# Performance work log

Measured on AMD Instinct MI355X. Metric: run time of the kernel, lower is better.

The kernel has to match this reference:

```python
import jax, jax.numpy as jnp
import numpy as np

EMBED_DIM = 1024
NUM_HEADS = 16
HEAD_DIM = EMBED_DIM // NUM_HEADS
CHUNK_SIZE = 10
LEFT_CONTEXT = 25
RIGHT_CONTEXT = 0
NEG_INF = -1e30  # stands in for float('-inf') additive mask, safe under softmax


def chunk_attention_mask(seq_len: int) -> jnp.ndarray:
    """Vectorized version of the per-row Python loop mask builder.
    Row i may attend to: its own chunk [chunk_start, chunk_end), the left
    context [i-left_context, chunk_start), and the right context
    [chunk_end, i+right_context+1)."""
    i = jnp.arange(seq_len)[:, None]
    j = jnp.arange(seq_len)[None, :]
    chunk_start = (i // CHUNK_SIZE) * CHUNK_SIZE
    chunk_end = jnp.minimum(chunk_start + CHUNK_SIZE, seq_len)
    in_chunk = (j >= chunk_start) & (j < chunk_end)
    in_left = (j >= i - LEFT_CONTEXT) & (j < chunk_start)
    in_right = (j >= chunk_end) & (j < jnp.minimum(seq_len, i + RIGHT_CONTEXT + 1))
    allowed = in_chunk | in_left | in_right
    return jnp.where(allowed, 0.0, NEG_INF).astype(jnp.float32)


def setup_inputs() -> dict:
    key = jax.random.key(0)
    ks = jax.random.split(key, 9)
    B, S, E = 2, 2048, EMBED_DIM
    s = 1.0 / np.sqrt(E)
    return {
        "hidden_states": jax.random.normal(ks[0], (B, S, E), jnp.float32),
        "Wq": jax.random.normal(ks[1], (E, E), jnp.float32) * s,
        "bq": jax.random.normal(ks[2], (E,), jnp.float32) * 0.02,
        "Wk": jax.random.normal(ks[3], (E, E), jnp.float32) * s,
        "bk": jax.random.normal(ks[4], (E,), jnp.float32) * 0.02,
        "Wv": jax.random.normal(ks[5], (E, E), jnp.float32) * s,
        "bv": jax.random.normal(ks[6], (E,), jnp.float32) * 0.02,
        "Wo": jax.random.normal(ks[7], (E, E), jnp.float32) * s,
        "bo": jax.random.normal(ks[8], (E,), jnp.float32) * 0.02,
    }


def reference(hidden_states, Wq, bq, Wk, bk, Wv, bv, Wo, bo):
    B, S, E = hidden_states.shape
    H, D = NUM_HEADS, HEAD_DIM
    scaling = D ** -0.5

    def proj(x, W, b):  # nn.Linear: x @ W.T + b, then split heads -> [B,H,S,D]
        y = jnp.einsum('bse,fe->bsf', x, W) + b
        return y.reshape(B, S, H, D).transpose(0, 2, 1, 3)

    q = proj(hidden_states, Wq, bq) * scaling
    k = proj(hidden_states, Wk, bk)
    v = proj(hidden_states, Wv, bv)

    scores = jnp.einsum('bhsd,bhtd->bhst', q, k)  # [B,H,S,S]
    scores = scores + chunk_attention_mask(S)[None, None]
    probs = jax.nn.softmax(scores, axis=-1)
    out = jnp.einsum('bhst,bhtd->bhsd', probs, v)  # [B,H,S,D]
    out = out.transpose(0, 2, 1, 3).reshape(B, S, E)
    out = jnp.einsum('bse,fe->bsf', out, Wo) + bo
    return out
```

## Files before the change

### kernel.cpp

```cpp
#include <hip/hip_runtime.h>
#include <stdint.h>

typedef unsigned short u16;
typedef __attribute__((ext_vector_type(8))) short short8;
typedef __attribute__((ext_vector_type(4))) short short4v;
typedef __attribute__((ext_vector_type(4))) float f32x4;

#define AS1 __attribute__((address_space(1)))
#define AS3 __attribute__((address_space(3)))

__device__ __forceinline__ u16 f2bf(float f) {
  uint32_t x = __builtin_bit_cast(uint32_t, f);
  uint32_t r = (x + 0x7fffu + ((x >> 16) & 1u)) >> 16;
  return (u16)r;
}
__device__ __forceinline__ float bf2f(u16 u) {
  return __builtin_bit_cast(float, (uint32_t)u << 16);
}

__device__ __forceinline__ void conv8(const float* __restrict__ s, u16* __restrict__ d, float sc) {
  float4 a = *(const float4*)s;
  float4 b = *(const float4*)(s + 4);
  union { u16 u[8]; uint4 v; } pk;
  pk.u[0] = f2bf(a.x * sc); pk.u[1] = f2bf(a.y * sc); pk.u[2] = f2bf(a.z * sc); pk.u[3] = f2bf(a.w * sc);
  pk.u[4] = f2bf(b.x * sc); pk.u[5] = f2bf(b.y * sc); pk.u[6] = f2bf(b.z * sc); pk.u[7] = f2bf(b.w * sc);
  *(uint4*)d = pk.v;
}
__device__ __forceinline__ void copy8f(const float* __restrict__ s, float* __restrict__ d, float sc) {
  float4 a = *(const float4*)s;
  float4 b = *(const float4*)(s + 4);
  a.x *= sc; a.y *= sc; a.z *= sc; a.w *= sc;
  b.x *= sc; b.y *= sc; b.z *= sc; b.w *= sc;
  *(float4*)d = a; *(float4*)(d + 4) = b;
}

__global__ void pack_kernel(const float* __restrict__ X,
                            const float* __restrict__ Wq, const float* __restrict__ bq,
                            const float* __restrict__ Wk, const float* __restrict__ bk,
                            const float* __restrict__ Wv, const float* __restrict__ bv,
                            const float* __restrict__ Wo,
                            u16* __restrict__ Xbf, u16* __restrict__ Wcat,
                            u16* __restrict__ Wobf, float* __restrict__ bcat) {
  int t = blockIdx.x * blockDim.x + threadIdx.x;
  if (t < 524288) { conv8(X + (size_t)t * 8, Xbf + (size_t)t * 8, 1.f); return; }
  t -= 524288;
  if (t < 131072) { conv8(Wq + (size_t)t * 8, Wcat + (size_t)t * 8, 0.125f); return; }
  t -= 131072;
  if (t < 131072) { conv8(Wk + (size_t)t * 8, Wcat + 1048576 + (size_t)t * 8, 1.f); return; }
  t -= 131072;
  if (t < 131072) { conv8(Wv + (size_t)t * 8, Wcat + 2097152 + (size_t)t * 8, 1.f); return; }
  t -= 131072;
  if (t < 131072) { conv8(Wo + (size_t)t * 8, Wobf + (size_t)t * 8, 1.f); return; }
  t -= 131072;
  if (t < 128) { copy8f(bq + t * 8, bcat + t * 8, 0.125f); return; }
  t -= 128;
  if (t < 128) { copy8f(bk + t * 8, bcat + 1024 + t * 8, 1.f); return; }
  t -= 128;
  if (t < 128) { copy8f(bv + t * 8, bcat + 2048 + t * 8, 1.f); return; }
}

template <int BN, bool OUT_BF16>
__global__ __launch_bounds__(512)
void gemm_bt(const u16* __restrict__ A, const u16* __restrict__ Bt,
             const float* __restrict__ bias, u16* __restrict__ Cbf,
             float* __restrict__ Cf, int M, int N, int K) {
  constexpr int SEG_A = 8;
  constexpr int SEG_B = BN / 16;
  constexpr int NSEG = SEG_A + SEG_B;
  constexpr int NWN = BN / 32;
  constexpr int NWM = 8 / NWN;
  constexpr int MI = 128 / (NWM * 16);
  __shared__ u16 As[2][128 * 32];
  __shared__ u16 Bs[2][BN * 32];
  const int wv = threadIdx.x >> 6;
  const int lane = threadIdx.x & 63;
  const int bm = blockIdx.x, bn = blockIdx.y;
  const int wm = wv / NWN, wn = wv % NWN;
  const int lrow = lane & 15, quad = lane >> 4;

  f32x4 acc[MI][2];
#pragma unroll
  for (int i = 0; i < MI; ++i)
#pragma unroll
    for (int j = 0; j < 2; ++j) acc[i][j] = (f32x4){0.f, 0.f, 0.f, 0.f};

  const long arow = (long)bm * 128;
  const long brow = (long)bn * BN;
  const int srow = lane >> 2;
  const int scol = ((lane & 3) ^ ((lane >> 3) & 3)) * 8;
  const int swz = (quad ^ ((lrow >> 1) & 3)) * 8;

  auto stage = [&](int nb, int k0) {
#pragma unroll
    for (int it = 0; it < 2; ++it) {
      const int s = wv + it * 8;
      if (s < NSEG) {
        const u16* g;
        u16* l;
        if (s < SEG_A) {
          g = A + (arow + s * 16 + srow) * K + k0 + scol;
          l = (u16*)As[nb] + s * 512;
        } else {
          g = Bt + (brow + (s - SEG_A) * 16 + srow) * K + k0 + scol;
          l = (u16*)Bs[nb] + (s - SEG_A) * 512;
        }
        __builtin_amdgcn_global_load_lds((AS1 void*)g, (AS3 void*)l, 16, 0, 0);
      }
    }
  };

  stage(0, 0);
  int cur = 0;
  for (int k0 = 0; k0 < K; k0 += 32) {
    __syncthreads();
    if (k0 + 32 < K) stage(cur ^ 1, k0 + 32);

    short8 af[MI], bfr[2];
#pragma unroll
    for (int mi = 0; mi < MI; ++mi)
      af[mi] = *(const short8*)(As[cur] + (wm * (MI * 16) + mi * 16 + lrow) * 32 + swz);
#pragma unroll
    for (int ni = 0; ni < 2; ++ni)
      bfr[ni] = *(const short8*)(Bs[cur] + (wn * 32 + ni * 16 + lrow) * 32 + swz);
#pragma unroll
    for (int mi = 0; mi < MI; ++mi)
#pragma unroll
      for (int ni = 0; ni < 2; ++ni)
        acc[mi][ni] = __builtin_amdgcn_mfma_f32_16x16x32_bf16(af[mi], bfr[ni], acc[mi][ni], 0, 0, 0);
    cur ^= 1;
  }

#pragma unroll
  for (int mi = 0; mi < MI; ++mi) {
#pragma unroll
    for (int ni = 0; ni < 2; ++ni) {
      const int col = bn * BN + wn * 32 + ni * 16 + lrow;
      const float bv = bias[col];
#pragma unroll
      for (int r = 0; r < 4; ++r) {
        const int row = bm * 128 + wm * (MI * 16) + mi * 16 + quad * 4 + r;
        const float v = acc[mi][ni][r] + bv;
        if constexpr (OUT_BF16) Cbf[(long)row * N + col] = f2bf(v);
        else Cf[(long)row * N + col] = v;
      }
    }
  }
}

#define NCH 205
#define VR_STRIDE 68
#define PB_STRIDE 72
#define WAVE_LDS (36 * VR_STRIDE + 16 * PB_STRIDE)

__global__ __launch_bounds__(256)
void attn_kernel(const u16* __restrict__ QKV, u16* __restrict__ ctx) {
  __shared__ __align__(16) u16 lds[4 * WAVE_LDS];
  const int wv = threadIdx.x >> 6;
  const int lane = threadIdx.x & 63;
  u16* Vr = lds + wv * WAVE_LDS;
  u16* Pb = Vr + 36 * VR_STRIDE;

  const int n = lane & 15, quad = lane >> 4;

  const int gw = blockIdx.x * 4 + wv;
  const int b = gw / (16 * NCH);
  int rem = gw - b * 16 * NCH;
  const int h = rem / NCH;
  const int c = rem - h * NCH;
  const int cs = c * 10;
  const int nq = min(10, 2048 - cs);
  const int w0 = max(cs - 25, 0);
  const int L = cs + nq - w0;

  const long base = ((long)b * 2048) * 3072 + (long)h * 64;

  for (int idx = lane; idx < (16 * PB_STRIDE) / 8; idx += 64)
    *(uint4*)(Pb + idx * 8) = (uint4){0, 0, 0, 0};

#pragma unroll
  for (int it = 0; it < 5; ++it) {
    const int slot = it * 64 + lane;
    const int j = slot >> 3, c8 = slot & 7;
    if (j < L) {
      const uint4 v = *(const uint4*)(QKV + base + (long)(w0 + j) * 3072 + 2048 + c8 * 8);
      u16* wp = Vr + j * VR_STRIDE + c8 * 8;
      *(uint2*)wp = (uint2){v.x, v.y};
      *(uint2*)(wp + 4) = (uint2){v.z, v.w};
    }
  }

  const int mclamp = min(n, nq - 1);
  const long qrow = base + (long)(cs + mclamp) * 3072;
  short8 aq0 = *(const short8*)(QKV + qrow + quad * 8);
  short8 aq1 = *(const short8*)(QKV + qrow + 32 + quad * 8);

  f32x4 sc[3];
#pragma unroll
  for (int t = 0; t < 3; ++t) {
    const int jj = min(16 * t + n, L - 1);
    const long krow = base + (long)(w0 + jj) * 3072 + 1024;
    short8 bk0 = *(const short8*)(QKV + krow + quad * 8);
    short8 bk1 = *(const short8*)(QKV + krow + 32 + quad * 8);
    f32x4 z = (f32x4){0.f, 0.f, 0.f, 0.f};
    z = __builtin_amdgcn_mfma_f32_16x16x32_bf16(aq0, bk0, z, 0, 0, 0);
    sc[t] = __builtin_amdgcn_mfma_f32_16x16x32_bf16(aq1, bk1, z, 0, 0, 0);
  }

#pragma unroll
  for (int r = 0; r < 4; ++r) {
    const int i = cs + quad * 4 + r;
    const int jlo = max(i - 25, 0) - w0;
    float v0 = (n >= jlo && n < L)      ? sc[0][r] : -1e30f;
    float v1 = (16 + n >= jlo && 16 + n < L) ? sc[1][r] : -1e30f;
    float v2 = (32 + n >= jlo && 32 + n < L) ? sc[2][r] : -1e30f;
    float m = fmaxf(v0, fmaxf(v1, v2));
#pragma unroll
    for (int off = 8; off > 0; off >>= 1) m = fmaxf(m, __shfl_xor(m, off));
    float p0 = __expf(v0 - m), p1 = __expf(v1 - m), p2 = __expf(v2 - m);
    float sum = p0 + p1 + p2;
#pragma unroll
    for (int off = 8; off > 0; off >>= 1) sum += __shfl_xor(sum, off);
    const float inv = 1.f / sum;
    u16* prow = Pb + (quad * 4 + r) * PB_STRIDE;
    prow[n]      = f2bf(p0 * inv);
    prow[16 + n] = f2bf(p1 * inv);
    prow[32 + n] = f2bf(p2 * inv);
  }

  short8 ap0 = *(const short8*)(Pb + n * PB_STRIDE + quad * 8);
  short8 ap1 = *(const short8*)(Pb + n * PB_STRIDE + 32 + quad * 8);
  const int icap = (L - 1) * VR_STRIDE;
  const int ib0 = (quad * 8) * VR_STRIDE;
  const int ib1 = ib0 + 32 * VR_STRIDE;
  f32x4 o[4];
#pragma unroll
  for (int dt = 0; dt < 4; ++dt) {
    const u16* colp = Vr + dt * 16 + n;
    short8 bv0, bv1;
#pragma unroll
    for (int e = 0; e < 8; ++e) {
      int i0 = ib0 + e * VR_STRIDE; i0 = i0 < icap ? i0 : icap;
      int i1 = ib1 + e * VR_STRIDE; i1 = i1 < icap ? i1 : icap;
      bv0[e] = (short)colp[i0];
      bv1[e] = (short)colp[i1];
    }
    f32x4 z = (f32x4){0.f, 0.f, 0.f, 0.f};
    z = __builtin_amdgcn_mfma_f32_16x16x32_bf16(ap0, bv0, z, 0, 0, 0);
    o[dt] = __builtin_amdgcn_mfma_f32_16x16x32_bf16(ap1, bv1, z, 0, 0, 0);
  }

#pragma unroll
  for (int dt = 0; dt < 4; ++dt) {
#pragma unroll
    for (int r = 0; r < 4; ++r) {
      const int row = quad * 4 + r;
      if (row < nq)
        ctx[((long)b * 2048 + cs + row) * 1024 + h * 64 + dt * 16 + n] = f2bf(o[dt][r]);
    }
  }
}

extern "C" void kernel_launch(void* const* d_in, const int* in_sizes, int n_in,
                              void* d_out, int out_size, void* d_ws, size_t ws_size,
                              hipStream_t stream) {
  const float* X  = (const float*)d_in[0];
  const float* Wq = (const float*)d_in[1];
  const float* bq = (const float*)d_in[2];
  const float* Wk = (const float*)d_in[3];
  const float* bk = (const float*)d_in[4];
  const float* Wv = (const float*)d_in[5];
  const float* bv = (const float*)d_in[6];
  const float* Wo = (const float*)d_in[7];
  const float* bo = (const float*)d_in[8];
  float* out = (float*)d_out;

  char* ws = (char*)d_ws;
  u16* Xbf   = (u16*)(ws);
  u16* Wcat  = (u16*)(ws + 8388608);
  u16* Wobf  = (u16*)(ws + 14680064);
  float* bcat = (float*)(ws + 16777216);
  u16* QKV   = (u16*)(ws + 16789504);
  u16* ctx   = (u16*)(ws + 41955328);

  pack_kernel<<<4098, 256, 0, stream>>>(X, Wq, bq, Wk, bk, Wv, bv, Wo, Xbf, Wcat, Wobf, bcat);
  gemm_bt<128, true ><<<dim3(32, 24), 512, 0, stream>>>(Xbf, Wcat, bcat, QKV, nullptr, 4096, 3072, 1024);
  attn_kernel<<<1640, 256, 0, stream>>>(QKV, ctx);
  gemm_bt<64, false><<<dim3(32, 16), 512, 0, stream>>>(ctx, Wobf, bo, nullptr, out, 4096, 1024, 1024);
}
```

Measured before the change: 157.5 us.

## Replace QKV projection GEMM with 256x256-tile pipelined MFMA kernel

Adds a dedicated GEMM for the fused QKV projection. It uses 256x256 output tiles and double-buffered LDS filled by direct global-to-LDS loads. The main loop is split into four sub-phases, each interleaving prefetch of later k-slices with MFMA bursts under raised wave priority. Larger tiles cut global traffic per FLOP and barrier overhead, but the grid shrinks to 192 blocks, which may leave compute units idle. The epilogue still uses scalar bf16 stores.

```diff
diff --git a/kernel.cpp b/kernel.cpp
--- a/kernel.cpp
+++ b/kernel.cpp
@@ -59,6 +59,152 @@
   if (t < 128) { copy8f(bv + t * 8, bcat + 2048 + t * 8, 1.f); return; }
 }
 
+__global__ __launch_bounds__(512, 1)
+void gemm256(const u16* __restrict__ A, const u16* __restrict__ Bt,
+             const float* __restrict__ bias, u16* __restrict__ Cbf,
+             int N, int K) {
+  __shared__ u16 Al[2][2][256 * 32];
+  __shared__ u16 Bl[2][2][256 * 32];
+  const int wv = threadIdx.x >> 6;
+  const int lane = threadIdx.x & 63;
+  const int bm = blockIdx.x, bn = blockIdx.y;
+  const int wm = wv >> 2, wn = wv & 3;
+  const int lrow = lane & 15, quad = lane >> 4;
+
+  f32x4 acc[8][4];
+#pragma unroll
+  for (int i = 0; i < 8; ++i)
+#pragma unroll
+    for (int j = 0; j < 4; ++j) acc[i][j] = (f32x4){0.f, 0.f, 0.f, 0.f};
+
+  const long arow = (long)bm * 256;
+  const long brow = (long)bn * 256;
+  const int srow = lane >> 2;
+  const int scol = ((lane & 3) ^ ((lane >> 3) & 3)) * 8;
+  const int swz = (quad ^ ((lrow >> 1) & 3)) * 8;
+
+  auto stageA = [&](int tt, int kk) {
+#pragma unroll
+    for (int it = 0; it < 2; ++it) {
+      const int s = wv * 2 + it;
+      const u16* g = A + (arow + s * 16 + srow) * K + tt * 64 + kk * 32 + scol;
+      u16* l = &Al[tt & 1][kk][s * 512];
+      __builtin_amdgcn_global_load_lds((AS1 void*)g, (AS3 void*)l, 16, 0, 0);
+    }
+  };
+  auto stageB = [&](int tt, int kk) {
+#pragma unroll
+    for (int it = 0; it < 2; ++it) {
+      const int s = wv * 2 + it;
+      const u16* g = Bt + (brow + s * 16 + srow) * K + tt * 64 + kk * 32 + scol;
+      u16* l = &Bl[tt & 1][kk][s * 512];
+      __builtin_amdgcn_global_load_lds((AS1 void*)g, (AS3 void*)l, 16, 0, 0);
+    }
+  };
+
+  stageA(0, 0); stageB(0, 0); stageA(0, 1); stageB(0, 1); stageA(1, 0); stageB(1, 0);
+  asm volatile("s_waitcnt vmcnt(4)" ::: "memory");
+  __builtin_amdgcn_s_barrier();
+
+  const int NT = K >> 6;
+  for (int t = 0; t < NT; ++t) {
+    const int p = t & 1;
+    short8 af[4], bf[4];
+
+#pragma unroll
+    for (int mi = 0; mi < 4; ++mi)
+      af[mi] = *(const short8*)(&Al[p][0][(wm * 128 + mi * 16 + lrow) * 32 + swz]);
+#pragma unroll
+    for (int ni = 0; ni < 4; ++ni)
+      bf[ni] = *(const short8*)(&Bl[p][0][(wn * 64 + ni * 16 + lrow) * 32 + swz]);
+    if (t + 1 < NT) stageA(t + 1, 1);
+    __builtin_amdgcn_s_barrier();
+    asm volatile("s_waitcnt lgkmcnt(0)" ::: "memory");
+    __builtin_amdgcn_sched_barrier(0);
+    __builtin_amdgcn_s_setprio(1);
+#pragma unroll
+    for (int mi = 0; mi < 4; ++mi)
+#pragma unroll
+      for (int ni = 0; ni < 4; ++ni)
+        acc[mi][ni] = __builtin_amdgcn_mfma_f32_16x16x32_bf16(af[mi], bf[ni], acc[mi][ni], 0, 0, 0);
+    __builtin_amdgcn_s_setprio(0);
+    __builtin_amdgcn_s_barrier();
+
+#pragma unroll
+    for (int mi = 0; mi < 4; ++mi)
+      af[mi] = *(const short8*)(&Al[p][0][(wm * 128 + 64 + mi * 16 + lrow) * 32 + swz]);
+#pragma unroll
+    for (int ni = 0; ni < 4; ++ni)
+      bf[ni] = *(const short8*)(&Bl[p][0][(wn * 64 + ni * 16 + lrow) * 32 + swz]);
+    if (t + 1 < NT) stageB(t + 1, 1);
+    __builtin_amdgcn_s_barrier();
+    asm volatile("s_waitcnt lgkmcnt(0)" ::: "memory");
+    __builtin_amdgcn_sched_barrier(0);
+    __builtin_amdgcn_s_setprio(1);
+#pragma unroll
+    for (int mi = 0; mi < 4; ++mi)
+#pragma unroll
+      for (int ni = 0; ni < 4; ++ni)
+        acc[4 + mi][ni] = __builtin_amdgcn_mfma_f32_16x16x32_bf16(af[mi], bf[ni], acc[4 + mi][ni], 0, 0, 0);
+    __builtin_amdgcn_s_setprio(0);
+    __builtin_amdgcn_s_barrier();
+
+#pragma unroll
+    for (int mi = 0; mi < 4; ++mi)
+      af[mi] = *(const short8*)(&Al[p][1][(wm * 128 + mi * 16 + lrow) * 32 + swz]);
+#pragma unroll
+    for (int ni = 0; ni < 4; ++ni)
+      bf[ni] = *(const short8*)(&Bl[p][1][(wn * 64 + ni * 16 + lrow) * 32 + swz]);
+    if (t + 2 < NT) stageA(t + 2, 0);
+    __builtin_amdgcn_s_barrier();
+    asm volatile("s_waitcnt lgkmcnt(0)" ::: "memory");
+    __builtin_amdgcn_sched_barrier(0);
+    __builtin_amdgcn_s_setprio(1);
+#pragma unroll
+    for (int mi = 0; mi < 4; ++mi)
+#pragma unroll
+      for (int ni = 0; ni < 4; ++ni)
+        acc[mi][ni] = __builtin_amdgcn_mfma_f32_16x16x32_bf16(af[mi], bf[ni], acc[mi][ni], 0, 0, 0);
+    __builtin_amdgcn_s_setprio(0);
+    __builtin_amdgcn_s_barrier();
+
+#pragma unroll
+    for (int mi = 0; mi < 4; ++mi)
+      af[mi] = *(const short8*)(&Al[p][1][(wm * 128 + 64 + mi * 16 + lrow) * 32 + swz]);
+#pragma unroll
+    for (int ni = 0; ni < 4; ++ni)
+      bf[ni] = *(const short8*)(&Bl[p][1][(wn * 64 + ni * 16 + lrow) * 32 + swz]);
+    if (t + 2 < NT) stageB(t + 2, 0);
+    __builtin_amdgcn_s_barrier();
+    asm volatile("s_waitcnt lgkmcnt(0)" ::: "memory");
+    __builtin_amdgcn_sched_barrier(0);
+    __builtin_amdgcn_s_setprio(1);
+#pragma unroll
+    for (int mi = 0; mi < 4; ++mi)
+#pragma unroll
+      for (int ni = 0; ni < 4; ++ni)
+        acc[4 + mi][ni] = __builtin_amdgcn_mfma_f32_16x16x32_bf16(af[mi], bf[ni], acc[4 + mi][ni], 0, 0, 0);
+    __builtin_amdgcn_s_setprio(0);
+    if (t + 2 < NT) asm volatile("s_waitcnt vmcnt(4)" ::: "memory");
+    else            asm volatile("s_waitcnt vmcnt(0)" ::: "memory");
+    __builtin_amdgcn_s_barrier();
+  }
+
+#pragma unroll
+  for (int fi = 0; fi < 8; ++fi) {
+#pragma unroll
+    for (int ni = 0; ni < 4; ++ni) {
+      const int col = bn * 256 + wn * 64 + ni * 16 + lrow;
+      const float bv = bias[col];
+#pragma unroll
+      for (int r = 0; r < 4; ++r) {
+        const int row = bm * 256 + wm * 128 + fi * 16 + quad * 4 + r;
+        Cbf[(long)row * N + col] = f2bf(acc[fi][ni][r] + bv);
+      }
+    }
+  }
+}
+
 template <int BN, bool OUT_BF16>
 __global__ __launch_bounds__(512)
 void gemm_bt(const u16* __restrict__ A, const u16* __restrict__ Bt,
@@ -283,7 +429,7 @@
   u16* ctx   = (u16*)(ws + 41955328);
 
   pack_kernel<<<4098, 256, 0, stream>>>(X, Wq, bq, Wk, bk, Wv, bv, Wo, Xbf, Wcat, Wobf, bcat);
-  gemm_bt<128, true ><<<dim3(32, 24), 512, 0, stream>>>(Xbf, Wcat, bcat, QKV, nullptr, 4096, 3072, 1024);
+  gemm256<<<dim3(16, 12), 512, 0, stream>>>(Xbf, Wcat, bcat, QKV, 3072, 1024);
   attn_kernel<<<1640, 256, 0, stream>>>(QKV, ctx);
   gemm_bt<64, false><<<dim3(32, 16), 512, 0, stream>>>(ctx, Wobf, bo, nullptr, out, 4096, 1024, 1024);
 }
```

Result: slower. 161.6 us (+2.7%).

## Tile attention by 16-query groups instead of 10-row chunks

Applied to the files above, without the earlier changes.

Each attention wave now handles 16 consecutive queries, which may span two chunks, instead of one 10-query chunk that left 6 of the 16 MFMA rows unused. The key window grows to at most 50 rows, so the kernel uses a fourth score tile, a larger LDS V buffer and a per-row upper mask bound taken from each query's own chunk end. Removing the idle rows cuts the total wave count and drops the P buffer zeroing and the partial-row store guards. In exchange, each wave does more score MFMAs and loads more V rows.

```diff
diff --git a/kernel.cpp b/kernel.cpp
--- a/kernel.cpp
+++ b/kernel.cpp
@@ -147,10 +147,9 @@
   }
 }
 
-#define NCH 205
 #define VR_STRIDE 68
 #define PB_STRIDE 72
-#define WAVE_LDS (36 * VR_STRIDE + 16 * PB_STRIDE)
+#define WAVE_LDS (50 * VR_STRIDE + 16 * PB_STRIDE)
 
 __global__ __launch_bounds__(256)
 void attn_kernel(const u16* __restrict__ QKV, u16* __restrict__ ctx) {
@@ -158,27 +157,24 @@
   const int wv = threadIdx.x >> 6;
   const int lane = threadIdx.x & 63;
   u16* Vr = lds + wv * WAVE_LDS;
-  u16* Pb = Vr + 36 * VR_STRIDE;
+  u16* Pb = Vr + 50 * VR_STRIDE;
 
   const int n = lane & 15, quad = lane >> 4;
 
   const int gw = blockIdx.x * 4 + wv;
-  const int b = gw / (16 * NCH);
-  int rem = gw - b * 16 * NCH;
-  const int h = rem / NCH;
-  const int c = rem - h * NCH;
-  const int cs = c * 10;
-  const int nq = min(10, 2048 - cs);
-  const int w0 = max(cs - 25, 0);
-  const int L = cs + nq - w0;
+  const int b = gw >> 11;
+  const int rem = gw & 2047;
+  const int h = rem >> 7;
+  const int g = rem & 127;
+  const int q0 = g * 16;
+  const int w0 = max(q0 - 25, 0);
+  const int end = min(((q0 + 15) / 10) * 10 + 10, 2048);
+  const int L = end - w0;
 
   const long base = ((long)b * 2048) * 3072 + (long)h * 64;
 
-  for (int idx = lane; idx < (16 * PB_STRIDE) / 8; idx += 64)
-    *(uint4*)(Pb + idx * 8) = (uint4){0, 0, 0, 0};
-
-#pragma unroll
-  for (int it = 0; it < 5; ++it) {
+#pragma unroll
+  for (int it = 0; it < 7; ++it) {
     const int slot = it * 64 + lane;
     const int j = slot >> 3, c8 = slot & 7;
     if (j < L) {
@@ -189,14 +185,13 @@
     }
   }
 
-  const int mclamp = min(n, nq - 1);
-  const long qrow = base + (long)(cs + mclamp) * 3072;
+  const long qrow = base + (long)(q0 + n) * 3072;
   short8 aq0 = *(const short8*)(QKV + qrow + quad * 8);
   short8 aq1 = *(const short8*)(QKV + qrow + 32 + quad * 8);
 
-  f32x4 sc[3];
-#pragma unroll
-  for (int t = 0; t < 3; ++t) {
+  f32x4 sc[4];
+#pragma unroll
+  for (int t = 0; t < 4; ++t) {
     const int jj = min(16 * t + n, L - 1);
     const long krow = base + (long)(w0 + jj) * 3072 + 1024;
     short8 bk0 = *(const short8*)(QKV + krow + quad * 8);
@@ -208,16 +203,18 @@
 
 #pragma unroll
   for (int r = 0; r < 4; ++r) {
-    const int i = cs + quad * 4 + r;
+    const int i = q0 + quad * 4 + r;
     const int jlo = max(i - 25, 0) - w0;
-    float v0 = (n >= jlo && n < L)      ? sc[0][r] : -1e30f;
-    float v1 = (16 + n >= jlo && 16 + n < L) ? sc[1][r] : -1e30f;
-    float v2 = (32 + n >= jlo && 32 + n < L) ? sc[2][r] : -1e30f;
-    float m = fmaxf(v0, fmaxf(v1, v2));
+    const int jhi = min((i / 10) * 10 + 10, 2048) - w0;
+    float v0 = (n >= jlo && n < jhi)           ? sc[0][r] : -1e30f;
+    float v1 = (16 + n >= jlo && 16 + n < jhi) ? sc[1][r] : -1e30f;
+    float v2 = (32 + n >= jlo && 32 + n < jhi) ? sc[2][r] : -1e30f;
+    float v3 = (48 + n >= jlo && 48 + n < jhi) ? sc[3][r] : -1e30f;
+    float m = fmaxf(fmaxf(v0, v1), fmaxf(v2, v3));
 #pragma unroll
     for (int off = 8; off > 0; off >>= 1) m = fmaxf(m, __shfl_xor(m, off));
-    float p0 = __expf(v0 - m), p1 = __expf(v1 - m), p2 = __expf(v2 - m);
-    float sum = p0 + p1 + p2;
+    float p0 = __expf(v0 - m), p1 = __expf(v1 - m), p2 = __expf(v2 - m), p3 = __expf(v3 - m);
+    float sum = (p0 + p1) + (p2 + p3);
 #pragma unroll
     for (int off = 8; off > 0; off >>= 1) sum += __shfl_xor(sum, off);
     const float inv = 1.f / sum;
@@ -225,6 +222,7 @@
     prow[n]      = f2bf(p0 * inv);
     prow[16 + n] = f2bf(p1 * inv);
     prow[32 + n] = f2bf(p2 * inv);
+    prow[48 + n] = f2bf(p3 * inv);
   }
 
   short8 ap0 = *(const short8*)(Pb + n * PB_STRIDE + quad * 8);
@@ -254,8 +252,7 @@
 #pragma unroll
     for (int r = 0; r < 4; ++r) {
       const int row = quad * 4 + r;
-      if (row < nq)
-        ctx[((long)b * 2048 + cs + row) * 1024 + h * 64 + dt * 16 + n] = f2bf(o[dt][r]);
+      ctx[((long)b * 2048 + q0 + row) * 1024 + h * 64 + dt * 16 + n] = f2bf(o[dt][r]);
     }
   }
 }
@@ -284,6 +281,6 @@
 
   pack_kernel<<<4098, 256, 0, stream>>>(X, Wq, bq, Wk, bk, Wv, bv, Wo, Xbf, Wcat, Wobf, bcat);
   gemm_bt<128, true ><<<dim3(32, 24), 512, 0, stream>>>(Xbf, Wcat, bcat, QKV, nullptr, 4096, 3072, 1024);
-  attn_kernel<<<1640, 256, 0, stream>>>(QKV, ctx);
+  attn_kernel<<<1024, 256, 0, stream>>>(QKV, ctx);
   gemm_bt<64, false><<<dim3(32, 16), 512, 0, stream>>>(ctx, Wobf, bo, nullptr, out, 4096, 1024, 1024);
 }
```

Result: faster. 152.6 us, median of 2 (-3.1%).
